# Kernel tuning notes

Measured on AMD Instinct MI355X. Metric: run time of the kernel, lower is better.

## Reference

```python
import jax, jax.numpy as jnp
import numpy as np
from jax import lax

DIM = 512
E = 16
NC = 1000
ROUTER_TEMP = 1.0


def _conv(x, w, b):
    # NCHW conv, 3x3, SAME padding (matches nn.Conv2d(padding=1))
    y = lax.conv_general_dilated(x, w, (1, 1), 'SAME',
                                 dimension_numbers=('NCHW', 'OIHW', 'NCHW'))
    return y + b[None, :, None, None]


def _avgpool2(x):
    B, C, H, W = x.shape
    return x.reshape(B, C, H // 2, 2, W // 2, 2).mean(axis=(3, 5))


def setup_inputs() -> dict:
    key = jax.random.key(0)
    ks = jax.random.split(key, 12)
    B, C, H, W = 128, 3, 128, 128

    def init(k, shape, fan_in):
        return jax.random.normal(k, shape, jnp.float32) * (1.0 / np.sqrt(fan_in))

    return {
        'x': jax.random.normal(ks[0], (B, C, H, W), jnp.float32),
        'conv1_w': init(ks[1], (32, 3, 3, 3), 3 * 9),   'conv1_b': jnp.zeros((32,), jnp.float32),
        'conv2_w': init(ks[2], (32, 32, 3, 3), 32 * 9), 'conv2_b': jnp.zeros((32,), jnp.float32),
        'conv3_w': init(ks[3], (64, 32, 3, 3), 32 * 9), 'conv3_b': jnp.zeros((64,), jnp.float32),
        'conv4_w': init(ks[4], (64, 64, 3, 3), 64 * 9), 'conv4_b': jnp.zeros((64,), jnp.float32),
        'proj_w': init(ks[5], (64, DIM), 64),           'proj_b': jnp.zeros((DIM,), jnp.float32),
        'router_w': init(ks[6], (DIM, E), DIM),         'router_b': jnp.zeros((E,), jnp.float32),
        # stacked expert MLPs: Linear(dim,dim) -> ReLU -> Linear(dim,num_classes)
        'w1': init(ks[7], (E, DIM, DIM), DIM), 'b1': jnp.zeros((E, DIM), jnp.float32),
        'w2': init(ks[8], (E, DIM, NC), DIM),  'b2': jnp.zeros((E, NC), jnp.float32),
    }


def reference(x, conv1_w, conv1_b, conv2_w, conv2_b, conv3_w, conv3_b,
              conv4_w, conv4_b, proj_w, proj_b, router_w, router_b,
              w1, b1, w2, b2):
    # ---- Encoder ----
    h = jax.nn.relu(_conv(x, conv1_w, conv1_b))
    h = jax.nn.relu(_conv(h, conv2_w, conv2_b))
    h = _avgpool2(h)
    h = jax.nn.relu(_conv(h, conv3_w, conv3_b))
    h = _avgpool2(h)
    h = jax.nn.relu(_conv(h, conv4_w, conv4_b))
    h = h.mean(axis=(2, 3))                      # AdaptiveAvgPool2d(1) -> [B, 64]
    z = h @ proj_w + proj_b                      # [B, DIM]

    # ---- Router (top-1 gating) ----
    gate_logits = (z @ router_w + router_b) / ROUTER_TEMP   # [B, E]
    gate_probs = jax.nn.softmax(gate_logits, axis=-1)
    top1 = jnp.argmax(gate_probs, axis=-1)                  # [B] int
    B = z.shape[0]

    counts = lax.stop_gradient(
        jnp.zeros((E,), jnp.float32).at[top1].add(1.0) / B)
    importance = gate_probs.mean(axis=0)                    # [E]
    aux_loss = E * jnp.sum(counts * importance)

    # ---- Expert dispatch: gather per-token expert weights (top-1 hard routing) ----
    h1 = jax.nn.relu(jnp.einsum('bd,bdk->bk', z, w1[top1]) + b1[top1])   # [B, DIM]
    logits = jnp.einsum('bd,bdk->bk', h1, w2[top1]) + b2[top1]           # [B, NC]

    return logits, aux_loss, lax.stop_gradient(counts), lax.stop_gradient(importance)
```

## Files before the change

### kernel.cpp

```cpp
#include <hip/hip_runtime.h>
#include <math.h>

typedef unsigned short ushort_t;
typedef short short4x __attribute__((ext_vector_type(4)));
typedef short short8 __attribute__((ext_vector_type(8)));
typedef float f32x16 __attribute__((ext_vector_type(16)));

#define MFMA32(A,B,C) __builtin_amdgcn_mfma_f32_32x32x16_bf16(A,B,C,0,0,0)

__device__ __forceinline__ ushort_t f2bf(float f) {
    union { float f; unsigned u; } c; c.f = f;
    unsigned u = c.u;
    unsigned r = (u + 0x7FFFu + ((u >> 16) & 1u)) >> 16;
    return (ushort_t)r;
}

__device__ __forceinline__ unsigned pk2bf(float lo, float hi) {
    unsigned r;
    asm("v_cvt_pk_bf16_f32 %0, %1, %2" : "=v"(r) : "v"(lo), "v"(hi));
    return r;
}

template<int CTRL>
__device__ __forceinline__ float dppadd(float v) {
    int p = __builtin_amdgcn_mov_dpp(__builtin_bit_cast(int, v), CTRL, 0xF, 0xF, true);
    return v + __builtin_bit_cast(float, p);
}

__global__ __launch_bounds__(256) void k_wcvt(
    const float* __restrict__ c1w, const float* __restrict__ c2w,
    const float* __restrict__ c3w, const float* __restrict__ c4w,
    ushort_t* __restrict__ c1f, ushort_t* __restrict__ w2f,
    ushort_t* __restrict__ w3f, ushort_t* __restrict__ w4f,
    float* __restrict__ feat, float* __restrict__ tail)
{
    if (blockIdx.x == 33) {
        for (int i = threadIdx.x; i < 8192; i += 256) feat[i] = 0.f;
        if (threadIdx.x < 33) tail[threadIdx.x] = 0.f;
        return;
    }
    int r = blockIdx.x * 256 + threadIdx.x;
    int lane = r & 63, m = lane & 31, g = (lane >> 5) & 1;
    if (r < 1152) {
        int f = r >> 6, tau = f >> 1, h = f & 1, ky = tau / 3, kx = tau % 3;
        #pragma unroll
        for (int j = 0; j < 8; ++j) {
            int ic = h * 16 + g * 8 + j;
            w2f[r * 8 + j] = f2bf(c2w[((m * 32 + ic) * 3 + ky) * 3 + kx]);
        }
    } else if (r < 3456) {
        int rr = r - 1152;
        int f = rr >> 6;
        int ot = f / 18, fl = f % 18, tau = fl >> 1, h = fl & 1, ky = tau / 3, kx = tau % 3;
        int oc = ot * 32 + m;
        #pragma unroll
        for (int j = 0; j < 8; ++j) {
            int ic = h * 16 + g * 8 + j;
            w3f[rr * 8 + j] = f2bf(c3w[((oc * 32 + ic) * 3 + ky) * 3 + kx]);
        }
    } else if (r < 8064) {
        int rr = r - 3456;
        int f = rr >> 6;
        int ot = f / 36, fl = f % 36, tau = fl >> 2, h = fl & 3, ky = tau / 3, kx = tau % 3;
        int oc = ot * 32 + m;
        #pragma unroll
        for (int j = 0; j < 8; ++j) {
            int ic = h * 16 + g * 8 + j;
            w4f[rr * 8 + j] = f2bf(c4w[((oc * 64 + ic) * 3 + ky) * 3 + kx]);
        }
    } else if (r < 8256) {
        int rr = r - 8064;
        int f = rr >> 6;
        #pragma unroll
        for (int j = 0; j < 8; ++j) {
            int k = f * 16 + g * 8 + j;
            int p = k >> 2, c = k & 3;
            ushort_t v = 0;
            if (p < 9 && c < 3)
                v = f2bf(c1w[(m * 3 + c) * 9 + p]);
            c1f[rr * 8 + j] = v;
        }
    }
}

__global__ __launch_bounds__(512, 4) void k_c12(
    const float* __restrict__ x,
    const ushort_t* __restrict__ c1f, const float* __restrict__ c1b,
    const ushort_t* __restrict__ w2f, const float* __restrict__ c2b,
    ushort_t* __restrict__ a2)
{
    __shared__ __align__(16) ushort_t xs[1600];
    __shared__ __align__(16) ushort_t a1s[324 * 40];
    __shared__ float c2bs[32], c1bs[32];
    const int t = threadIdx.x;
    const int bx = blockIdx.x, by = blockIdx.y, b = blockIdx.z;
    const int ox0 = bx * 16, oy0 = by * 16;

    if (t < 32) { c2bs[t] = c2b[t]; c1bs[t] = c1b[t]; }
    for (int i = t; i < 400; i += 512) {
        int yy = i / 20, xx = i % 20;
        int gy = oy0 - 2 + yy, gx = ox0 - 2 + xx;
        float v0 = 0.f, v1 = 0.f, v2 = 0.f;
        if (gy >= 0 && gy < 128 && gx >= 0 && gx < 128) {
            const float* px = x + ((size_t)(b * 3) * 128 + gy) * 128 + gx;
            v0 = px[0]; v1 = px[16384]; v2 = px[32768];
        }
        uint2 pk;
        pk.x = pk2bf(v0, v1);
        pk.y = pk2bf(v2, 0.f);
        *(uint2*)&xs[i * 4] = pk;
    }

    const int wave = t >> 6, lane = t & 63;
    const int n = lane & 31, g = lane >> 5;

    short8 a1f0 = *(const short8*)(c1f + lane * 8);
    short8 a1f1 = *(const short8*)(c1f + (64 + lane) * 8);
    short8 a1f2 = *(const short8*)(c1f + (128 + lane) * 8);
    __syncthreads();

    float cb1[16];
    #pragma unroll
    for (int qd = 0; qd < 4; ++qd)
        #pragma unroll
        for (int jj = 0; jj < 4; ++jj)
            cb1[qd * 4 + jj] = c1bs[qd * 8 + 4 * g + jj];

    for (int grp = wave; grp < 11; grp += 8) {
        int q = grp * 32 + n;
        bool qv = q < 324;
        int qc = qv ? q : 0;
        int cy = qc / 18, cx = qc % 18;
        int gy = oy0 - 1 + cy, gx = ox0 - 1 + cx;
        bool inimg = qv && gy >= 0 && gy < 128 && gx >= 0 && gx < 128;
        int base = (cy * 20 + cx) * 4;

        short4x q0 = *(const short4x*)&xs[base + (g ? 8 : 0)];
        short4x q1 = *(const short4x*)&xs[base + (g ? 80 : 4)];
        short4x q2 = *(const short4x*)&xs[base + (g ? 160 : 84)];
        short4x q3 = *(const short4x*)&xs[base + (g ? 164 : 88)];
        short4x q4 = *(const short4x*)&xs[base + 168];

        short8 b0 = __builtin_shufflevector(q0, q1, 0, 1, 2, 3, 4, 5, 6, 7);
        short8 b1 = __builtin_shufflevector(q2, q3, 0, 1, 2, 3, 4, 5, 6, 7);
        short8 b2 = __builtin_shufflevector(q4, q4, 0, 1, 2, 3, 0, 1, 2, 3);

        f32x16 acc;
        #pragma unroll
        for (int i = 0; i < 16; ++i) acc[i] = 0.f;
        acc = MFMA32(a1f0, b0, acc);
        acc = MFMA32(a1f1, b1, acc);
        acc = MFMA32(a1f2, b2, acc);

        if (qv) {
            const int mq = (q >> 3) & 3;
            ushort_t* cellp = &a1s[q * 40 + 4 * g];
            #pragma unroll
            for (int qd = 0; qd < 4; ++qd) {
                float v0 = fmaxf(acc[qd * 4 + 0] + cb1[qd * 4 + 0], 0.f);
                float v1 = fmaxf(acc[qd * 4 + 1] + cb1[qd * 4 + 1], 0.f);
                float v2 = fmaxf(acc[qd * 4 + 2] + cb1[qd * 4 + 2], 0.f);
                float v3 = fmaxf(acc[qd * 4 + 3] + cb1[qd * 4 + 3], 0.f);
                uint2 pk;
                pk.x = inimg ? pk2bf(v0, v1) : 0u;
                pk.y = inimg ? pk2bf(v2, v3) : 0u;
                *(uint2*)&cellp[8 * (qd ^ mq)] = pk;
            }
        }
    }
    __syncthreads();

    const int x2 = (n >> 2) * 2 + (n & 1);
    const int y2 = wave * 2 + ((n >> 1) & 1);

    short8 af[18];
    #pragma unroll
    for (int f = 0; f < 18; ++f)
        af[f] = *(const short8*)(w2f + (f * 64 + lane) * 8);

    f32x16 acc;
    #pragma unroll
    for (int i = 0; i < 16; ++i) acc[i] = 0.f;

    #pragma unroll
    for (int tau = 0; tau < 9; ++tau) {
        int dy = tau / 3, dx = tau % 3;
        int cell = (y2 + dy) * 18 + (x2 + dx);
        int mq = (cell >> 3) & 3;
        const ushort_t* bb = &a1s[cell * 40];
        int o0 = (g ^ mq) * 8;
        short8 b0 = *(const short8*)(bb + o0);
        short8 b1 = *(const short8*)(bb + (o0 ^ 16));
        acc = MFMA32(af[tau * 2 + 0], b0, acc);
        acc = MFMA32(af[tau * 2 + 1], b1, acc);
    }

    float pv[16];
    #pragma unroll
    for (int r = 0; r < 16; ++r) {
        float v = fmaxf(acc[r] + c2bs[(r & 3) + 8 * (r >> 2) + 4 * g], 0.f);
        v = dppadd<0xB1>(v);
        v = dppadd<0x4E>(v);
        pv[r] = v * 0.25f;
    }
    if ((n & 3) == 0) {
        const int poy = by * 8 + wave, pox = bx * 8 + (n >> 2);
        ushort_t* dst = &a2[(((size_t)b * 64 + poy) * 64 + pox) * 32 + 4 * g];
        #pragma unroll
        for (int qd = 0; qd < 4; ++qd) {
            uint2 pk;
            pk.x = pk2bf(pv[qd * 4 + 0], pv[qd * 4 + 1]);
            pk.y = pk2bf(pv[qd * 4 + 2], pv[qd * 4 + 3]);
            *(uint2*)&dst[8 * qd] = pk;
        }
    }
}

__global__ __launch_bounds__(512, 4) void k_c3(
    const ushort_t* __restrict__ a2, const ushort_t* __restrict__ w3f,
    const float* __restrict__ c3b, ushort_t* __restrict__ a3)
{
    __shared__ __align__(16) ushort_t s[324 * 40];
    __shared__ float bs[64];
    const int t = threadIdx.x;
    const int bx = blockIdx.x, by = blockIdx.y, b = blockIdx.z;
    const int x0 = bx * 16, y0 = by * 16;
    if (t < 64) bs[t] = c3b[t];
    for (int idx = t; idx < 1296; idx += 512) {
        int cell = idx >> 2, part = idx & 3;
        int cy = cell / 18, cx = cell % 18;
        int gy = y0 - 1 + cy, gx = x0 - 1 + cx;
        uint4 v = make_uint4(0, 0, 0, 0);
        if (gy >= 0 && gy < 64 && gx >= 0 && gx < 64)
            v = *(const uint4*)(a2 + (((size_t)b * 64 + gy) * 64 + gx) * 32 + part * 8);
        int mq = (cell >> 3) & 3;
        *(uint4*)(&s[cell * 40 + (part ^ mq) * 8]) = v;
    }
    __syncthreads();

    const int wave = t >> 6, lane = t & 63;
    const int n = lane & 31, g = lane >> 5;
    const int x3 = (n >> 2) * 2 + (n & 1);
    const int y3 = wave * 2 + ((n >> 1) & 1);

    f32x16 acc0, acc1;
    #pragma unroll
    for (int i = 0; i < 16; ++i) { acc0[i] = 0.f; acc1[i] = 0.f; }

    #pragma unroll
    for (int tau = 0; tau < 9; ++tau) {
        int dy = tau / 3, dx = tau % 3;
        int cell = (y3 + dy) * 18 + (x3 + dx);
        int mq = (cell >> 3) & 3;
        const ushort_t* bb = &s[cell * 40];
        int o0 = (g ^ mq) * 8;
        short8 b0 = *(const short8*)(bb + o0);
        short8 b1 = *(const short8*)(bb + (o0 ^ 16));
        short8 a00 = *(const short8*)(w3f + ((tau * 2 + 0) * 64 + lane) * 8);
        short8 a01 = *(const short8*)(w3f + ((tau * 2 + 1) * 64 + lane) * 8);
        short8 a10 = *(const short8*)(w3f + (((18 + tau * 2) + 0) * 64 + lane) * 8);
        short8 a11 = *(const short8*)(w3f + (((18 + tau * 2) + 1) * 64 + lane) * 8);
        acc0 = MFMA32(a00, b0, acc0);
        acc0 = MFMA32(a01, b1, acc0);
        acc1 = MFMA32(a10, b0, acc1);
        acc1 = MFMA32(a11, b1, acc1);
    }

    const int poy = by * 8 + wave, pox = bx * 8 + (n >> 2);
    ushort_t* dst = &a3[(((size_t)b * 32 + poy) * 32 + pox) * 64 + 4 * g];
    #pragma unroll
    for (int ot = 0; ot < 2; ++ot) {
        const f32x16& ac = ot ? acc1 : acc0;
        float pv[16];
        #pragma unroll
        for (int r = 0; r < 16; ++r) {
            float v = fmaxf(ac[r] + bs[ot * 32 + (r & 3) + 8 * (r >> 2) + 4 * g], 0.f);
            v = dppadd<0xB1>(v);
            v = dppadd<0x4E>(v);
            pv[r] = v * 0.25f;
        }
        if ((n & 3) == 0) {
            #pragma unroll
            for (int qd = 0; qd < 4; ++qd) {
                uint2 pk;
                pk.x = pk2bf(pv[qd * 4 + 0], pv[qd * 4 + 1]);
                pk.y = pk2bf(pv[qd * 4 + 2], pv[qd * 4 + 3]);
                *(uint2*)&dst[ot * 32 + 8 * qd] = pk;
            }
        }
    }
}

__global__ __launch_bounds__(512, 2) void k_c4(
    const ushort_t* __restrict__ a3, const ushort_t* __restrict__ w4f,
    const float* __restrict__ c4b, float* __restrict__ feat)
{
    __shared__ __align__(16) ushort_t s[324 * 72];
    __shared__ float bs[64];
    const int t = threadIdx.x;
    const int bx = blockIdx.x, by = blockIdx.y, b = blockIdx.z;
    const int x0 = bx * 16, y0 = by * 16;
    if (t < 64) bs[t] = c4b[t];
    for (int idx = t; idx < 2592; idx += 512) {
        int cell = idx >> 3, part = idx & 7;
        int cy = cell / 18, cx = cell % 18;
        int gy = y0 - 1 + cy, gx = x0 - 1 + cx;
        uint4 v = make_uint4(0, 0, 0, 0);
        if (gy >= 0 && gy < 32 && gx >= 0 && gx < 32)
            v = *(const uint4*)(a3 + (((size_t)b * 32 + gy) * 32 + gx) * 64 + part * 8);
        int mq = (cell >> 3) & 3;
        *(uint4*)(&s[cell * 72 + (part ^ mq) * 8]) = v;
    }
    __syncthreads();

    const int wave = t >> 6, lane = t & 63;
    const int n = lane & 31, g = lane >> 5;
    const int ry = n >> 4, rx = n & 15;
    const int y4 = wave * 2 + ry;

    f32x16 acc0, acc1;
    #pragma unroll
    for (int i = 0; i < 16; ++i) { acc0[i] = 0.f; acc1[i] = 0.f; }

    #pragma unroll
    for (int hp = 0; hp < 2; ++hp) {
        #pragma unroll
        for (int tau = 0; tau < 9; ++tau) {
            int dy = tau / 3, dx = tau % 3;
            int cell = (y4 + dy) * 18 + (rx + dx);
            int mq = (cell >> 3) & 3;
            const ushort_t* bb = &s[cell * 72];
            int o0 = ((4 * hp + g) ^ mq) * 8;
            short8 b0 = *(const short8*)(bb + o0);
            short8 b1 = *(const short8*)(bb + (o0 ^ 16));
            short8 a00 = *(const short8*)(w4f + ((tau * 4 + hp * 2 + 0) * 64 + lane) * 8);
            short8 a01 = *(const short8*)(w4f + ((tau * 4 + hp * 2 + 1) * 64 + lane) * 8);
            short8 a10 = *(const short8*)(w4f + ((36 + tau * 4 + hp * 2 + 0) * 64 + lane) * 8);
            short8 a11 = *(const short8*)(w4f + ((36 + tau * 4 + hp * 2 + 1) * 64 + lane) * 8);
            acc0 = MFMA32(a00, b0, acc0);
            acc0 = MFMA32(a01, b1, acc0);
            acc1 = MFMA32(a10, b0, acc1);
            acc1 = MFMA32(a11, b1, acc1);
        }
    }

    #pragma unroll
    for (int ot = 0; ot < 2; ++ot) {
        const f32x16& ac = ot ? acc1 : acc0;
        #pragma unroll
        for (int r = 0; r < 16; ++r) {
            int oc = ot * 32 + (r & 3) + 8 * (r >> 2) + 4 * g;
            float v = fmaxf(ac[r] + bs[oc], 0.f);
            v = dppadd<0xB1>(v);
            v = dppadd<0x4E>(v);
            v += __shfl_xor(v, 4);
            v += __shfl_xor(v, 8);
            v += __shfl_xor(v, 16);
            if ((lane & 31) == 0)
                atomicAdd(&feat[b * 64 + oc], v * (1.0f / 1024.0f));
        }
    }
}

__global__ __launch_bounds__(256) void k_router(
    const float* __restrict__ meanacc,
    const float* __restrict__ pw, const float* __restrict__ pb,
    const float* __restrict__ rw, const float* __restrict__ rb,
    ushort_t* __restrict__ zb, int* __restrict__ top1, float* __restrict__ tail)
{
    __shared__ float m[64];
    __shared__ float zs[512];
    __shared__ float part[256];
    __shared__ float gate[16];
    const int b = blockIdx.x, t = threadIdx.x;
    if (t < 64) m[t] = meanacc[b * 64 + t];
    __syncthreads();

    #pragma unroll
    for (int j = 0; j < 2; ++j) {
        int d = t + j * 256;
        float s = pb[d];
        for (int c = 0; c < 64; ++c) s += m[c] * pw[c * 512 + d];
        zs[d] = s;
        zb[b * 512 + d] = f2bf(s);
    }
    __syncthreads();
    {
        int e = t & 15, gg = t >> 4;
        float s = 0.f;
        for (int j = 0; j < 32; ++j) {
            int d = gg * 32 + j;
            s += zs[d] * rw[d * 16 + e];
        }
        part[t] = s;
    }
    __syncthreads();
    if (t < 16) {
        float s = rb[t];
        for (int gg = 0; gg < 16; ++gg) s += part[gg * 16 + t];
        gate[t] = s;
    }
    __syncthreads();
    if (t == 0) {
        float mx = gate[0];
        int am = 0;
        for (int e = 1; e < 16; ++e)
            if (gate[e] > mx) { mx = gate[e]; am = e; }
        float pr[16];
        float sum = 0.f;
        for (int e = 0; e < 16; ++e) { pr[e] = expf(gate[e] - mx); sum += pr[e]; }
        float inv = 1.f / sum;
        top1[b] = am;
        atomicAdd(&tail[1 + am], 1.0f / 128.0f);
        for (int e = 0; e < 16; ++e)
            atomicAdd(&tail[17 + e], pr[e] * inv * (1.0f / 128.0f));
    }
}

__global__ void k_sort(const int* __restrict__ top1, int* __restrict__ meta,
                       int* __restrict__ perm, float* __restrict__ tail)
{
    __shared__ int c[16], o[16], pos[128];
    const int t = threadIdx.x;
    if (t < 16) c[t] = 0;
    __syncthreads();
    int e = 0;
    if (t < 128) { e = top1[t]; pos[t] = atomicAdd(&c[e], 1); }
    __syncthreads();
    if (t == 0) {
        int s = 0;
        for (int i = 0; i < 16; ++i) { o[i] = s; s += c[i]; }
        int nt = 0;
        for (int i = 0; i < 16; ++i) {
            for (int r0 = 0; r0 < c[i]; r0 += 32) {
                meta[33 + nt] = i;
                meta[53 + nt] = o[i] + r0;
                int rem = c[i] - r0;
                meta[73 + nt] = rem < 32 ? rem : 32;
                ++nt;
            }
        }
        meta[32] = nt;
        for (int k = nt; k < 20; ++k) { meta[33 + k] = 0; meta[53 + k] = 0; meta[73 + k] = 0; }
        float s2 = 0.f;
        for (int i = 0; i < 16; ++i) s2 += tail[1 + i] * tail[17 + i];
        tail[0] = 16.0f * s2;
    }
    __syncthreads();
    if (t < 128) perm[o[e] + pos[t]] = t;
    if (t < 16) { meta[t] = c[t]; meta[16 + t] = o[t]; }
}

__global__ __launch_bounds__(64) void k_mlp1(
    const ushort_t* __restrict__ zb, const int* __restrict__ meta, const int* __restrict__ perm,
    const float* __restrict__ w1, const float* __restrict__ b1, ushort_t* __restrict__ h1b)
{
    const int ty = blockIdx.y;
    if (ty >= meta[32]) return;
    const int e = meta[33 + ty], ts = meta[53 + ty], rows = meta[73 + ty];
    const int n0 = blockIdx.x * 32;
    __shared__ __align__(16) ushort_t ws[32 * 520];
    __shared__ int tks[32];
    const int lane = threadIdx.x;
    const int mn = lane & 31, g = lane >> 5;

    if (lane < 32) tks[lane] = (lane < rows) ? perm[ts + lane] : -1;

    const float* Wg = w1 + ((size_t)e << 18) + n0;
    {
        const int cq = lane & 7, dg = lane >> 3;
        #pragma unroll 4
        for (int it = 0; it < 32; ++it) {
            int d = it * 16 + dg * 2;
            float4 va = *(const float4*)(Wg + (size_t)d * 512 + 4 * cq);
            float4 vb = *(const float4*)(Wg + (size_t)(d + 1) * 512 + 4 * cq);
            *(unsigned*)&ws[(4 * cq + 0) * 520 + d] = pk2bf(va.x, vb.x);
            *(unsigned*)&ws[(4 * cq + 1) * 520 + d] = pk2bf(va.y, vb.y);
            *(unsigned*)&ws[(4 * cq + 2) * 520 + d] = pk2bf(va.z, vb.z);
            *(unsigned*)&ws[(4 * cq + 3) * 520 + d] = pk2bf(va.w, vb.w);
        }
    }
    __syncthreads();

    const int tok_a = tks[mn] < 0 ? 0 : tks[mn];
    const ushort_t* za = zb + (size_t)tok_a * 512;

    f32x16 acc;
    #pragma unroll
    for (int i = 0; i < 16; ++i) acc[i] = 0.f;

    #pragma unroll 4
    for (int kt = 0; kt < 16; ++kt) {
        int k0 = kt * 32;
        short8 a0 = *(const short8*)(za + k0 + g * 8);
        short8 a1 = *(const short8*)(za + k0 + 16 + g * 8);
        short8 b0 = *(const short8*)(&ws[mn * 520 + k0 + g * 8]);
        short8 b1 = *(const short8*)(&ws[mn * 520 + k0 + 16 + g * 8]);
        acc = MFMA32(a0, b0, acc);
        acc = MFMA32(a1, b1, acc);
    }

    const float bias = b1[e * 512 + n0 + mn];
    #pragma unroll
    for (int r = 0; r < 16; ++r) {
        int mrow = (r & 3) + 8 * (r >> 2) + 4 * g;
        int tok = tks[mrow];
        if (tok >= 0) {
            float v = fmaxf(acc[r] + bias, 0.f);
            h1b[(size_t)tok * 512 + n0 + mn] = f2bf(v);
        }
    }
}

__global__ __launch_bounds__(64) void k_mlp2(
    const ushort_t* __restrict__ h1b, const int* __restrict__ meta, const int* __restrict__ perm,
    const float* __restrict__ w2, const float* __restrict__ b2, float* __restrict__ out)
{
    const int ty = blockIdx.y;
    if (ty >= meta[32]) return;
    const int e = meta[33 + ty], ts = meta[53 + ty], rows = meta[73 + ty];
    const int n0 = blockIdx.x * 32;
    __shared__ __align__(16) ushort_t ws[32 * 520];
    __shared__ int tks[32];
    const int lane = threadIdx.x;
    const int mn = lane & 31, g = lane >> 5;

    if (lane < 32) tks[lane] = (lane < rows) ? perm[ts + lane] : -1;

    const float* Wg = w2 + (size_t)e * 512000 + n0;
    {
        const int cq = lane & 7, dg = lane >> 3;
        const bool cut = (n0 == 992) && (cq >= 2);
        #pragma unroll 4
        for (int it = 0; it < 32; ++it) {
            int d = it * 16 + dg * 2;
            float4 va = make_float4(0.f, 0.f, 0.f, 0.f), vb = va;
            if (!cut) {
                va = *(const float4*)(Wg + (size_t)d * 1000 + 4 * cq);
                vb = *(const float4*)(Wg + (size_t)(d + 1) * 1000 + 4 * cq);
            }
            *(unsigned*)&ws[(4 * cq + 0) * 520 + d] = pk2bf(va.x, vb.x);
            *(unsigned*)&ws[(4 * cq + 1) * 520 + d] = pk2bf(va.y, vb.y);
            *(unsigned*)&ws[(4 * cq + 2) * 520 + d] = pk2bf(va.z, vb.z);
            *(unsigned*)&ws[(4 * cq + 3) * 520 + d] = pk2bf(va.w, vb.w);
        }
    }
    __syncthreads();

    const int tok_a = tks[mn] < 0 ? 0 : tks[mn];
    const ushort_t* ha = h1b + (size_t)tok_a * 512;

    f32x16 acc;
    #pragma unroll
    for (int i = 0; i < 16; ++i) acc[i] = 0.f;

    #pragma unroll 4
    for (int kt = 0; kt < 16; ++kt) {
        int k0 = kt * 32;
        short8 a0 = *(const short8*)(ha + k0 + g * 8);
        short8 a1 = *(const short8*)(ha + k0 + 16 + g * 8);
        short8 b0 = *(const short8*)(&ws[mn * 520 + k0 + g * 8]);
        short8 b1 = *(const short8*)(&ws[mn * 520 + k0 + 16 + g * 8]);
        acc = MFMA32(a0, b0, acc);
        acc = MFMA32(a1, b1, acc);
    }

    const int col = n0 + mn;
    if (col < 1000) {
        const float bias = b2[e * 1000 + col];
        #pragma unroll
        for (int r = 0; r < 16; ++r) {
            int mrow = (r & 3) + 8 * (r >> 2) + 4 * g;
            int tok = tks[mrow];
            if (tok >= 0)
                out[(size_t)tok * 1000 + col] = acc[r] + bias;
        }
    }
}

extern "C" void kernel_launch(void* const* d_in, const int* in_sizes, int n_in,
                              void* d_out, int out_size, void* d_ws, size_t ws_size,
                              hipStream_t stream)
{
    const float* x   = (const float*)d_in[0];
    const float* c1w = (const float*)d_in[1];
    const float* c1b = (const float*)d_in[2];
    const float* c2w = (const float*)d_in[3];
    const float* c2b = (const float*)d_in[4];
    const float* c3w = (const float*)d_in[5];
    const float* c3b = (const float*)d_in[6];
    const float* c4w = (const float*)d_in[7];
    const float* c4b = (const float*)d_in[8];
    const float* pw  = (const float*)d_in[9];
    const float* pb  = (const float*)d_in[10];
    const float* rw  = (const float*)d_in[11];
    const float* rb  = (const float*)d_in[12];
    const float* w1  = (const float*)d_in[13];
    const float* b1  = (const float*)d_in[14];
    const float* w2  = (const float*)d_in[15];
    const float* b2  = (const float*)d_in[16];

    float* out = (float*)d_out;
    float* tail = out + 128000;

    char* w = (char*)d_ws;
    ushort_t* a2   = (ushort_t*)(w);
    ushort_t* a3   = (ushort_t*)(w + 33554432);
    ushort_t* w2f  = (ushort_t*)(w + 50331648);
    ushort_t* w3f  = (ushort_t*)(w + 50350080);
    ushort_t* w4f  = (ushort_t*)(w + 50386944);
    ushort_t* c1f  = (ushort_t*)(w + 50460672);
    float*    feat = (float*)(w + 50464768);
    ushort_t* zb   = (ushort_t*)(w + 50497536);
    ushort_t* h1b  = (ushort_t*)(w + 50628608);
    int*      top1 = (int*)(w + 50759680);
    int*      meta = (int*)(w + 50760192);
    int*      perm = (int*)(w + 50760704);

    k_wcvt  <<<34, 256, 0, stream>>>(c1w, c2w, c3w, c4w, c1f, w2f, w3f, w4f, feat, tail);
    k_c12   <<<dim3(8, 8, 128), 512, 0, stream>>>(x, c1f, c1b, w2f, c2b, a2);
    k_c3    <<<dim3(4, 4, 128), 512, 0, stream>>>(a2, w3f, c3b, a3);
    k_c4    <<<dim3(2, 2, 128), 512, 0, stream>>>(a3, w4f, c4b, feat);
    k_router<<<128, 256, 0, stream>>>(feat, pw, pb, rw, rb, zb, top1, tail);
    k_sort  <<<1, 128, 0, stream>>>(top1, meta, perm, tail);
    k_mlp1  <<<dim3(16, 20), 64, 0, stream>>>(zb, meta, perm, w1, b1, h1b);
    k_mlp2  <<<dim3(32, 20), 64, 0, stream>>>(h1b, meta, perm, w2, b2, out);
}
```

Baseline: 194.0 us.

## Fold pool scales into weights, conv1 bias into MFMA, drop LDS XOR swizzle

Moves the avgpool 0.25 scales and the final 1/1024 mean into the bf16 conv weights and biases, which is valid because ReLU is positively homogeneous. The conv1 bias becomes part of the MFMA by setting the padding channel to 1 and storing the bias in the matching weight slot. The XOR-based LDS swizzle in the conv kernels is removed, which simplifies address arithmetic. In exchange, LDS bank conflicts may rise, and scaling weights before bf16 rounding changes numerics slightly.

```diff
diff --git a/kernel.cpp b/kernel.cpp
--- a/kernel.cpp
+++ b/kernel.cpp
@@ -28,8 +28,8 @@
 }
 
 __global__ __launch_bounds__(256) void k_wcvt(
-    const float* __restrict__ c1w, const float* __restrict__ c2w,
-    const float* __restrict__ c3w, const float* __restrict__ c4w,
+    const float* __restrict__ c1w, const float* __restrict__ c1b_,
+    const float* __restrict__ c2w, const float* __restrict__ c3w, const float* __restrict__ c4w,
     ushort_t* __restrict__ c1f, ushort_t* __restrict__ w2f,
     ushort_t* __restrict__ w3f, ushort_t* __restrict__ w4f,
     float* __restrict__ feat, float* __restrict__ tail)
@@ -46,7 +46,7 @@
         #pragma unroll
         for (int j = 0; j < 8; ++j) {
             int ic = h * 16 + g * 8 + j;
-            w2f[r * 8 + j] = f2bf(c2w[((m * 32 + ic) * 3 + ky) * 3 + kx]);
+            w2f[r * 8 + j] = f2bf(0.25f * c2w[((m * 32 + ic) * 3 + ky) * 3 + kx]);
         }
     } else if (r < 3456) {
         int rr = r - 1152;
@@ -56,7 +56,7 @@
         #pragma unroll
         for (int j = 0; j < 8; ++j) {
             int ic = h * 16 + g * 8 + j;
-            w3f[rr * 8 + j] = f2bf(c3w[((oc * 32 + ic) * 3 + ky) * 3 + kx]);
+            w3f[rr * 8 + j] = f2bf(0.25f * c3w[((oc * 32 + ic) * 3 + ky) * 3 + kx]);
         }
     } else if (r < 8064) {
         int rr = r - 3456;
@@ -66,18 +66,20 @@
         #pragma unroll
         for (int j = 0; j < 8; ++j) {
             int ic = h * 16 + g * 8 + j;
-            w4f[rr * 8 + j] = f2bf(c4w[((oc * 64 + ic) * 3 + ky) * 3 + kx]);
+            w4f[rr * 8 + j] = f2bf(0.0009765625f * c4w[((oc * 64 + ic) * 3 + ky) * 3 + kx]);
         }
     } else if (r < 8256) {
         int rr = r - 8064;
-        int f = rr >> 6;
+        int f1 = rr >> 6;
         #pragma unroll
         for (int j = 0; j < 8; ++j) {
-            int k = f * 16 + g * 8 + j;
+            int k = f1 * 16 + g * 8 + j;
             int p = k >> 2, c = k & 3;
             ushort_t v = 0;
             if (p < 9 && c < 3)
                 v = f2bf(c1w[(m * 3 + c) * 9 + p]);
+            else if (k == 3)
+                v = f2bf(c1b_[m]);
             c1f[rr * 8 + j] = v;
         }
     }
@@ -85,18 +87,18 @@
 
 __global__ __launch_bounds__(512, 4) void k_c12(
     const float* __restrict__ x,
-    const ushort_t* __restrict__ c1f, const float* __restrict__ c1b,
+    const ushort_t* __restrict__ c1f,
     const ushort_t* __restrict__ w2f, const float* __restrict__ c2b,
     ushort_t* __restrict__ a2)
 {
     __shared__ __align__(16) ushort_t xs[1600];
     __shared__ __align__(16) ushort_t a1s[324 * 40];
-    __shared__ float c2bs[32], c1bs[32];
+    __shared__ float c2bs[32];
     const int t = threadIdx.x;
     const int bx = blockIdx.x, by = blockIdx.y, b = blockIdx.z;
     const int ox0 = bx * 16, oy0 = by * 16;
 
-    if (t < 32) { c2bs[t] = c2b[t]; c1bs[t] = c1b[t]; }
+    if (t < 32) c2bs[t] = 0.25f * c2b[t];
     for (int i = t; i < 400; i += 512) {
         int yy = i / 20, xx = i % 20;
         int gy = oy0 - 2 + yy, gx = ox0 - 2 + xx;
@@ -107,7 +109,7 @@
         }
         uint2 pk;
         pk.x = pk2bf(v0, v1);
-        pk.y = pk2bf(v2, 0.f);
+        pk.y = pk2bf(v2, 1.0f);
         *(uint2*)&xs[i * 4] = pk;
     }
 
@@ -118,13 +120,6 @@
     short8 a1f1 = *(const short8*)(c1f + (64 + lane) * 8);
     short8 a1f2 = *(const short8*)(c1f + (128 + lane) * 8);
     __syncthreads();
-
-    float cb1[16];
-    #pragma unroll
-    for (int qd = 0; qd < 4; ++qd)
-        #pragma unroll
-        for (int jj = 0; jj < 4; ++jj)
-            cb1[qd * 4 + jj] = c1bs[qd * 8 + 4 * g + jj];
 
     for (int grp = wave; grp < 11; grp += 8) {
         int q = grp * 32 + n;
@@ -153,18 +148,17 @@
         acc = MFMA32(a1f2, b2, acc);
 
         if (qv) {
-            const int mq = (q >> 3) & 3;
-            ushort_t* cellp = &a1s[q * 40 + 4 * g];
+            ushort_t* dst = &a1s[q * 40 + 4 * g];
             #pragma unroll
             for (int qd = 0; qd < 4; ++qd) {
-                float v0 = fmaxf(acc[qd * 4 + 0] + cb1[qd * 4 + 0], 0.f);
-                float v1 = fmaxf(acc[qd * 4 + 1] + cb1[qd * 4 + 1], 0.f);
-                float v2 = fmaxf(acc[qd * 4 + 2] + cb1[qd * 4 + 2], 0.f);
-                float v3 = fmaxf(acc[qd * 4 + 3] + cb1[qd * 4 + 3], 0.f);
+                float v0 = fmaxf(acc[qd * 4 + 0], 0.f);
+                float v1 = fmaxf(acc[qd * 4 + 1], 0.f);
+                float v2 = fmaxf(acc[qd * 4 + 2], 0.f);
+                float v3 = fmaxf(acc[qd * 4 + 3], 0.f);
                 uint2 pk;
                 pk.x = inimg ? pk2bf(v0, v1) : 0u;
                 pk.y = inimg ? pk2bf(v2, v3) : 0u;
-                *(uint2*)&cellp[8 * (qd ^ mq)] = pk;
+                *(uint2*)&dst[8 * qd] = pk;
             }
         }
     }
@@ -182,15 +176,12 @@
     #pragma unroll
     for (int i = 0; i < 16; ++i) acc[i] = 0.f;
 
+    const ushort_t* bbase = &a1s[(y2 * 18 + x2) * 40 + g * 8];
     #pragma unroll
     for (int tau = 0; tau < 9; ++tau) {
-        int dy = tau / 3, dx = tau % 3;
-        int cell = (y2 + dy) * 18 + (x2 + dx);
-        int mq = (cell >> 3) & 3;
-        const ushort_t* bb = &a1s[cell * 40];
-        int o0 = (g ^ mq) * 8;
-        short8 b0 = *(const short8*)(bb + o0);
-        short8 b1 = *(const short8*)(bb + (o0 ^ 16));
+        const int off = ((tau / 3) * 18 + (tau % 3)) * 40;
+        short8 b0 = *(const short8*)(bbase + off);
+        short8 b1 = *(const short8*)(bbase + off + 16);
         acc = MFMA32(af[tau * 2 + 0], b0, acc);
         acc = MFMA32(af[tau * 2 + 1], b1, acc);
     }
@@ -201,7 +192,7 @@
         float v = fmaxf(acc[r] + c2bs[(r & 3) + 8 * (r >> 2) + 4 * g], 0.f);
         v = dppadd<0xB1>(v);
         v = dppadd<0x4E>(v);
-        pv[r] = v * 0.25f;
+        pv[r] = v;
     }
     if ((n & 3) == 0) {
         const int poy = by * 8 + wave, pox = bx * 8 + (n >> 2);
@@ -225,7 +216,7 @@
     const int t = threadIdx.x;
     const int bx = blockIdx.x, by = blockIdx.y, b = blockIdx.z;
     const int x0 = bx * 16, y0 = by * 16;
-    if (t < 64) bs[t] = c3b[t];
+    if (t < 64) bs[t] = 0.25f * c3b[t];
     for (int idx = t; idx < 1296; idx += 512) {
         int cell = idx >> 2, part = idx & 3;
         int cy = cell / 18, cx = cell % 18;
@@ -233,8 +224,7 @@
         uint4 v = make_uint4(0, 0, 0, 0);
         if (gy >= 0 && gy < 64 && gx >= 0 && gx < 64)
             v = *(const uint4*)(a2 + (((size_t)b * 64 + gy) * 64 + gx) * 32 + part * 8);
-        int mq = (cell >> 3) & 3;
-        *(uint4*)(&s[cell * 40 + (part ^ mq) * 8]) = v;
+        *(uint4*)(&s[cell * 40 + part * 8]) = v;
     }
     __syncthreads();
 
@@ -247,15 +237,12 @@
     #pragma unroll
     for (int i = 0; i < 16; ++i) { acc0[i] = 0.f; acc1[i] = 0.f; }
 
+    const ushort_t* bbase = &s[(y3 * 18 + x3) * 40 + g * 8];
     #pragma unroll
     for (int tau = 0; tau < 9; ++tau) {
-        int dy = tau / 3, dx = tau % 3;
-        int cell = (y3 + dy) * 18 + (x3 + dx);
-        int mq = (cell >> 3) & 3;
-        const ushort_t* bb = &s[cell * 40];
-        int o0 = (g ^ mq) * 8;
-        short8 b0 = *(const short8*)(bb + o0);
-        short8 b1 = *(const short8*)(bb + (o0 ^ 16));
+        const int off = ((tau / 3) * 18 + (tau % 3)) * 40;
+        short8 b0 = *(const short8*)(bbase + off);
+        short8 b1 = *(const short8*)(bbase + off + 16);
         short8 a00 = *(const short8*)(w3f + ((tau * 2 + 0) * 64 + lane) * 8);
         short8 a01 = *(const short8*)(w3f + ((tau * 2 + 1) * 64 + lane) * 8);
         short8 a10 = *(const short8*)(w3f + (((18 + tau * 2) + 0) * 64 + lane) * 8);
@@ -277,7 +264,7 @@
             float v = fmaxf(ac[r] + bs[ot * 32 + (r & 3) + 8 * (r >> 2) + 4 * g], 0.f);
             v = dppadd<0xB1>(v);
             v = dppadd<0x4E>(v);
-            pv[r] = v * 0.25f;
+            pv[r] = v;
         }
         if ((n & 3) == 0) {
             #pragma unroll
@@ -300,7 +287,7 @@
     const int t = threadIdx.x;
     const int bx = blockIdx.x, by = blockIdx.y, b = blockIdx.z;
     const int x0 = bx * 16, y0 = by * 16;
-    if (t < 64) bs[t] = c4b[t];
+    if (t < 64) bs[t] = 0.0009765625f * c4b[t];
     for (int idx = t; idx < 2592; idx += 512) {
         int cell = idx >> 3, part = idx & 7;
         int cy = cell / 18, cx = cell % 18;
@@ -308,8 +295,7 @@
         uint4 v = make_uint4(0, 0, 0, 0);
         if (gy >= 0 && gy < 32 && gx >= 0 && gx < 32)
             v = *(const uint4*)(a3 + (((size_t)b * 32 + gy) * 32 + gx) * 64 + part * 8);
-        int mq = (cell >> 3) & 3;
-        *(uint4*)(&s[cell * 72 + (part ^ mq) * 8]) = v;
+        *(uint4*)(&s[cell * 72 + part * 8]) = v;
     }
     __syncthreads();
 
@@ -322,17 +308,14 @@
     #pragma unroll
     for (int i = 0; i < 16; ++i) { acc0[i] = 0.f; acc1[i] = 0.f; }
 
+    const ushort_t* bbase = &s[(y4 * 18 + rx) * 72 + g * 8];
     #pragma unroll
     for (int hp = 0; hp < 2; ++hp) {
         #pragma unroll
         for (int tau = 0; tau < 9; ++tau) {
-            int dy = tau / 3, dx = tau % 3;
-            int cell = (y4 + dy) * 18 + (rx + dx);
-            int mq = (cell >> 3) & 3;
-            const ushort_t* bb = &s[cell * 72];
-            int o0 = ((4 * hp + g) ^ mq) * 8;
-            short8 b0 = *(const short8*)(bb + o0);
-            short8 b1 = *(const short8*)(bb + (o0 ^ 16));
+            const int off = ((tau / 3) * 18 + (tau % 3)) * 72 + hp * 32;
+            short8 b0 = *(const short8*)(bbase + off);
+            short8 b1 = *(const short8*)(bbase + off + 16);
             short8 a00 = *(const short8*)(w4f + ((tau * 4 + hp * 2 + 0) * 64 + lane) * 8);
             short8 a01 = *(const short8*)(w4f + ((tau * 4 + hp * 2 + 1) * 64 + lane) * 8);
             short8 a10 = *(const short8*)(w4f + ((36 + tau * 4 + hp * 2 + 0) * 64 + lane) * 8);
@@ -357,7 +340,7 @@
             v += __shfl_xor(v, 8);
             v += __shfl_xor(v, 16);
             if ((lane & 31) == 0)
-                atomicAdd(&feat[b * 64 + oc], v * (1.0f / 1024.0f));
+                atomicAdd(&feat[b * 64 + oc], v);
         }
     }
 }
@@ -617,8 +600,8 @@
     int*      meta = (int*)(w + 50760192);
     int*      perm = (int*)(w + 50760704);
 
-    k_wcvt  <<<34, 256, 0, stream>>>(c1w, c2w, c3w, c4w, c1f, w2f, w3f, w4f, feat, tail);
-    k_c12   <<<dim3(8, 8, 128), 512, 0, stream>>>(x, c1f, c1b, w2f, c2b, a2);
+    k_wcvt  <<<34, 256, 0, stream>>>(c1w, c1b, c2w, c3w, c4w, c1f, w2f, w3f, w4f, feat, tail);
+    k_c12   <<<dim3(8, 8, 128), 512, 0, stream>>>(x, c1f, w2f, c2b, a2);
     k_c3    <<<dim3(4, 4, 128), 512, 0, stream>>>(a2, w3f, c3b, a3);
     k_c4    <<<dim3(2, 2, 128), 512, 0, stream>>>(a3, w4f, c4b, feat);
     k_router<<<128, 256, 0, stream>>>(feat, pw, pb, rw, rb, zb, top1, tail);
```

Measured after the change: 192.9 us, median of 3. No clear change (-0.5%).
